# Optimization experiments

Hardware: AMD Instinct MI355X
Metric: run time of the kernel (lower is better)

Reference implementation:

```python
import jax, jax.numpy as jnp
import numpy as np

DILATIONS = [2 ** i for i in range(10)] * 5  # dilation_depth=10, n_repeat=5 -> 50 layers
B, C_IN, L = 8, 256, 16384
N_RES, N_SKIP = 32, 512
FINAL_LEN = L - sum(DILATIONS)  # 16384 - 5115 = 11269 (valid causal convs shrink length)


def setup_inputs() -> dict:
    key = jax.random.key(0)
    ks = jax.random.split(key, 8)
    s = lambda k, shape, scale: jax.random.normal(k, shape, jnp.float32) * scale
    nl = len(DILATIONS)
    return {
        "x": s(ks[0], (B, C_IN, L), 1.0),
        "w_in": s(ks[1], (N_RES, C_IN, 1), 0.06),
        "b_in": jnp.zeros((N_RES,), jnp.float32),
        "w_sig": s(ks[2], (nl, N_RES, N_RES, 2), 0.12),
        "b_sig": jnp.zeros((nl, N_RES), jnp.float32),
        "w_tanh": s(ks[3], (nl, N_RES, N_RES, 2), 0.12),
        "b_tanh": jnp.zeros((nl, N_RES), jnp.float32),
        "w_skip": s(ks[4], (nl, N_SKIP, N_RES), 0.17),
        "b_skip": jnp.zeros((nl, N_SKIP), jnp.float32),
        "w_res": s(ks[5], (nl, N_RES, N_RES), 0.17),
        "b_res": jnp.zeros((nl, N_RES), jnp.float32),
        "w_post1": s(ks[6], (N_SKIP, N_SKIP, 1), 0.04),
        "b_post1": jnp.zeros((N_SKIP,), jnp.float32),
        "w_post2": s(ks[7], (C_IN, N_SKIP, 1), 0.04),
        "b_post2": jnp.zeros((C_IN,), jnp.float32),
    }


def _dconv(x, w, b, d):
    # valid (causal, no-pad) dilated conv1d; x: [B,C,L], w: [O,I,K]
    y = jax.lax.conv_general_dilated(
        x, w, window_strides=(1,), padding='VALID', rhs_dilation=(d,),
        dimension_numbers=('NCH', 'OIH', 'NCH'))
    return y + b[None, :, None]


def reference(x, w_in, b_in, w_sig, b_sig, w_tanh, b_tanh, w_skip, b_skip,
              w_res, b_res, w_post1, b_post1, w_post2, b_post2):
    out = _dconv(x, w_in, b_in, 1)  # [B, n_residue, L]
    skip_sum = jnp.zeros((x.shape[0], w_skip.shape[1], FINAL_LEN), x.dtype)
    for i, d in enumerate(DILATIONS):
        gate = jax.nn.sigmoid(_dconv(out, w_sig[i], b_sig[i], d)) \
             * jnp.tanh(_dconv(out, w_tanh[i], b_tanh[i], d))
        # 1x1 skip conv, immediately trimmed to the final length (same math as
        # torch's trim-at-the-end since only the last FINAL_LEN samples survive)
        skip = jnp.einsum('oc,bcl->bol', w_skip[i], gate[:, :, -FINAL_LEN:]) \
             + b_skip[i][None, :, None]
        skip_sum = skip_sum + skip
        res = jnp.einsum('oc,bcl->bol', w_res[i], gate) + b_res[i][None, :, None]
        out = res + out[:, :, -res.shape[2]:]
    h = jax.nn.elu(skip_sum)
    h = _dconv(h, w_post1, b_post1, 1)
    h = jax.nn.elu(h)
    return _dconv(h, w_post2, b_post2, 1)  # [B, 256, FINAL_LEN]
```

## Files before the change

### kernel.cpp

```cpp
#include <hip/hip_runtime.h>
#include <hip/hip_bf16.h>
#include <cstdio>
#include <cstdint>

#define BATCH 8
#define CIN 256
#define L0 16384
#define NRES 32
#define NSKIP 512
#define NL 50
#define FINAL_LEN 11269
#define NTROW 11392

typedef __attribute__((ext_vector_type(4))) float f32x4v;
typedef __attribute__((ext_vector_type(8))) short s16x8;
typedef __attribute__((ext_vector_type(4))) short s16x4;

__device__ __forceinline__ int SWS(int r, int s) {
    return s ^ (r & 3) ^ ((r >> 2) & 1);
}
__device__ __forceinline__ short f2bf(float f) {
    __hip_bfloat16 h = __float2bfloat16(f);
    return *reinterpret_cast<short*>(&h);
}
__device__ __forceinline__ void gload16(const void* g, void* l) {
    __builtin_amdgcn_global_load_lds(
        (const __attribute__((address_space(1))) unsigned int*)g,
        (__attribute__((address_space(3))) unsigned int*)l, 16, 0, 0);
}

__global__ void k_bias_sum(const float* __restrict__ b_skip, float* __restrict__ bsum) {
    int o = threadIdx.x;
    if (o < NSKIP) {
        float s = 0.f;
        for (int i = 0; i < NL; ++i) s += b_skip[i * NSKIP + o];
        bsum[o] = s;
    }
}

__global__ __launch_bounds__(256) void k_cvt_skip(const float* __restrict__ w, short* __restrict__ out) {
    int idx = blockIdx.x * 256 + threadIdx.x;
    if (idx >= NSKIP * NL) return;
    int o = idx % NSKIP, ly = idx / NSKIP;
    const float* src = w + ((size_t)ly * NSKIP + o) * NRES;
    size_t base = (size_t)o * (NL * NRES) + ly * NRES;
#pragma unroll
    for (int s = 0; s < 4; ++s) {
        s16x8 v;
#pragma unroll
        for (int j = 0; j < 8; ++j) v[j] = f2bf(src[s * 8 + j]);
        *reinterpret_cast<s16x8*>(out + base + SWS(o & 7, s) * 8) = v;
    }
}

__global__ __launch_bounds__(256) void k_cvt_mat(const float* __restrict__ w, short* __restrict__ out, int M) {
    int idx = blockIdx.x * 256 + threadIdx.x;
    if (idx >= M * 16) return;
    int m = idx >> 4, kc = idx & 15;
    const float* src = w + (size_t)m * 512 + kc * 32;
    size_t base = (size_t)m * 512 + kc * 32;
#pragma unroll
    for (int s = 0; s < 4; ++s) {
        s16x8 v;
#pragma unroll
        for (int j = 0; j < 8; ++j) v[j] = f2bf(src[s * 8 + j]);
        *reinterpret_cast<s16x8*>(out + base + SWS(m & 7, s) * 8) = v;
    }
}

__global__ __launch_bounds__(256) void k_cvt_w(
    const float* __restrict__ ws, const float* __restrict__ wt, const float* __restrict__ wr,
    short* __restrict__ Wc, short* __restrict__ Wres) {
    int idx = blockIdx.x * 256 + threadIdx.x;
    if (idx < NL * 64 * 64) {
        int k = idx & 63, o = (idx >> 6) & 63, i = idx >> 12;
        int c = k & 31, tap = k >> 5;
        float v = (o < 32) ? ws[((i * NRES + o) * NRES + c) * 2 + tap]
                           : wt[((i * NRES + (o - 32)) * NRES + c) * 2 + tap];
        Wc[idx] = f2bf(v);
    } else {
        int j = idx - NL * 64 * 64;
        if (j < NL * 32 * 32) Wres[j] = f2bf(wr[j]);
    }
}

__global__ __launch_bounds__(256) void k_zero_tail(short* __restrict__ gT) {
    int i = blockIdx.x * 256 + threadIdx.x;
    const int per_b = (NTROW - FINAL_LEN) * 200;
    if (i >= BATCH * per_b) return;
    int b = i / per_b, r = i % per_b;
    int row = FINAL_LEN + r / 200, c = r % 200;
    s16x8 z = {0, 0, 0, 0, 0, 0, 0, 0};
    *reinterpret_cast<s16x8*>(gT + ((size_t)b * NTROW + row) * (NL * NRES) + c * 8) = z;
}

__global__ __launch_bounds__(256) void k_conv_in(
    const float* __restrict__ x, const float* __restrict__ w,
    const float* __restrict__ bias, float* __restrict__ out, short* __restrict__ outH) {
    const int b = blockIdx.y;
    const int t = blockIdx.x * 256 + threadIdx.x;
    float acc[NRES];
#pragma unroll
    for (int o = 0; o < NRES; ++o) acc[o] = bias[o];
    const float* xp = x + (size_t)b * CIN * L0 + t;
    for (int c = 0; c < CIN; ++c) {
        float xv = xp[(size_t)c * L0];
#pragma unroll
        for (int o = 0; o < NRES; ++o) acc[o] = fmaf(w[o * CIN + c], xv, acc[o]);
    }
    float* op = out + (size_t)b * NRES * L0 + t;
#pragma unroll
    for (int o = 0; o < NRES; ++o) op[(size_t)o * L0] = acc[o];
    short* hp = outH + ((size_t)b * L0 + t) * NRES;
#pragma unroll
    for (int s = 0; s < 4; ++s) {
        s16x8 v;
#pragma unroll
        for (int j = 0; j < 8; ++j) v[j] = f2bf(acc[s * 8 + j]);
        *reinterpret_cast<s16x8*>(hp + s * 8) = v;
    }
}

__global__ __launch_bounds__(256) void k_layer_mfma(
    const float* __restrict__ srcF, const short* __restrict__ srcH,
    float* __restrict__ dstF, short* __restrict__ dstH,
    short* __restrict__ gout,
    const short* __restrict__ Wc,
    const short* __restrict__ Wr,
    const float* __restrict__ bsig, const float* __restrict__ btan,
    const float* __restrict__ bres, int d, int out_len) {
    const int tid = threadIdx.x;
    const int l = tid & 63, w = tid >> 6;
    const int lr = l & 15, lg = l >> 4;
    const int b = blockIdx.y;
    const int t0w = blockIdx.x * 256 + w * 64;
    const int t0g = out_len - FINAL_LEN;

    __shared__ short gsm[4][64][40];
    __shared__ short hsm[4][64][40];

    s16x8 aW[4][2];
#pragma unroll
    for (int mf = 0; mf < 4; ++mf)
#pragma unroll
        for (int kf = 0; kf < 2; ++kf)
            aW[mf][kf] = *reinterpret_cast<const s16x8*>(&Wc[(mf * 16 + lr) * 64 + kf * 32 + lg * 8]);
    s16x8 aR[2];
#pragma unroll
    for (int mf = 0; mf < 2; ++mf)
        aR[mf] = *reinterpret_cast<const s16x8*>(&Wr[(mf * 16 + lr) * 32 + lg * 8]);

    float bs[2][4], bt[2][4], br[2][4];
#pragma unroll
    for (int mf = 0; mf < 2; ++mf)
#pragma unroll
        for (int j = 0; j < 4; ++j) {
            int o = mf * 16 + lg * 4 + j;
            bs[mf][j] = bsig[o]; bt[mf][j] = btan[o]; br[mf][j] = bres[o];
        }

    const float* sF = srcF + (size_t)b * NRES * L0;
    const short* sH = srcH + (size_t)b * L0 * NRES;
    float* dF = dstF + (size_t)b * NRES * L0;

#pragma unroll 1
    for (int nf = 0; nf < 4; ++nf) {
        const int tl = nf * 16 + lr;
        const int t = t0w + tl;
        const int tc = t < out_len ? t : (out_len - 1);
        s16x8 bx0 = *reinterpret_cast<const s16x8*>(&sH[(size_t)tc * NRES + lg * 8]);
        s16x8 bx1 = *reinterpret_cast<const s16x8*>(&sH[(size_t)(tc + d) * NRES + lg * 8]);

        f32x4v acc[4];
#pragma unroll
        for (int mf = 0; mf < 4; ++mf) acc[mf] = {0.f, 0.f, 0.f, 0.f};
#pragma unroll
        for (int mf = 0; mf < 4; ++mf) {
            acc[mf] = __builtin_amdgcn_mfma_f32_16x16x32_bf16(aW[mf][0], bx0, acc[mf], 0, 0, 0);
            acc[mf] = __builtin_amdgcn_mfma_f32_16x16x32_bf16(aW[mf][1], bx1, acc[mf], 0, 0, 0);
        }

#pragma unroll
        for (int mf = 0; mf < 2; ++mf) {
            s16x4 gq;
#pragma unroll
            for (int j = 0; j < 4; ++j) {
                float Ps = acc[mf][j] + bs[mf][j];
                float Pt = acc[mf + 2][j] + bt[mf][j];
                float sg = 1.f / (1.f + __expf(-Ps));
                float e2 = __expf(2.f * Pt);
                float th = 1.f - 2.f / (e2 + 1.f);
                gq[j] = f2bf(sg * th);
            }
            *reinterpret_cast<s16x4*>(&gsm[w][tl][mf * 16 + lg * 4]) = gq;
        }
        __syncthreads();

        s16x8 bg = *reinterpret_cast<const s16x8*>(&gsm[w][tl][lg * 8]);
        f32x4v accR[2];
#pragma unroll
        for (int mf = 0; mf < 2; ++mf) {
            accR[mf] = {0.f, 0.f, 0.f, 0.f};
            accR[mf] = __builtin_amdgcn_mfma_f32_16x16x32_bf16(aR[mf], bg, accR[mf], 0, 0, 0);
        }

        if (t < out_len) {
#pragma unroll
            for (int mf = 0; mf < 2; ++mf) {
                s16x4 hq;
#pragma unroll
                for (int j = 0; j < 4; ++j) {
                    int o = mf * 16 + lg * 4 + j;
                    float v = accR[mf][j] + br[mf][j] + sF[(size_t)o * L0 + t + d];
                    dF[(size_t)o * L0 + t] = v;
                    hq[j] = f2bf(v);
                }
                *reinterpret_cast<s16x4*>(&hsm[w][tl][mf * 16 + lg * 4]) = hq;
            }
        }
    }
    __syncthreads();

    short* dH = dstH + (size_t)b * L0 * NRES;
#pragma unroll
    for (int k = 0; k < 4; ++k) {
        int r = k * 16 + (l >> 2);
        int t = t0w + r;
        int c = l & 3;
        if (t < out_len) {
            s16x8 hv = *reinterpret_cast<const s16x8*>(&hsm[w][r][c * 8]);
            *reinterpret_cast<s16x8*>(&dH[(size_t)t * NRES + c * 8]) = hv;
            if (t >= t0g) {
                int tg = t - t0g;
                s16x8 gv = *reinterpret_cast<const s16x8*>(&gsm[w][r][c * 8]);
                *reinterpret_cast<s16x8*>(
                    &gout[((size_t)b * NTROW + tg) * (NL * NRES) + SWS(tg & 7, c) * 8]) = gv;
            }
        }
    }
}

template <int KTOT, bool DOELU, int OUTMODE>
__global__ __launch_bounds__(256) void k_mm(
    const short* __restrict__ A, const float* __restrict__ bias,
    const short* __restrict__ B, short* __restrict__ outS,
    float* __restrict__ outF, int Mtot) {
    const int tid = threadIdx.x;
    const int l = tid & 63, w = tid >> 6;
    const int t0 = blockIdx.x * 128;
    const int m0 = blockIdx.y * 128;
    const int bb = blockIdx.z;

    __shared__ __attribute__((aligned(16))) char Asm_[2][8192];
    __shared__ __attribute__((aligned(16))) char Bsm_[2][8192];

    const char* Ag = (const char*)A;
    const char* Bg = (const char*)B + (size_t)bb * NTROW * (KTOT * 2);

    const int rstage = w * 16 + (l >> 2);
    const char* a0 = Ag + (size_t)(m0 + rstage) * (KTOT * 2) + (l & 3) * 16;
    const char* a1 = a0 + (size_t)64 * (KTOT * 2);
    const char* b0 = Bg + (size_t)(t0 + rstage) * (KTOT * 2) + (l & 3) * 16;
    const char* b1 = b0 + (size_t)64 * (KTOT * 2);

    const int wm = (w >> 1) * 64, wn = (w & 1) * 64;
    const int slotSw = ((l >> 4) ^ (l & 3) ^ ((l >> 2) & 1)) * 16;
    const int aoff = (wm + (l & 15)) * 64 + slotSw;
    const int boff = (wn + (l & 15)) * 64 + slotSw;

    f32x4v acc[4][4];
#pragma unroll
    for (int i = 0; i < 4; ++i)
#pragma unroll
        for (int j = 0; j < 4; ++j) acc[i][j] = {0.f, 0.f, 0.f, 0.f};

    constexpr int NKT = KTOT / 32;
    gload16(a0, &Asm_[0][w * 1024]);
    gload16(a1, &Asm_[0][4096 + w * 1024]);
    gload16(b0, &Bsm_[0][w * 1024]);
    gload16(b1, &Bsm_[0][4096 + w * 1024]);
    __syncthreads();

    for (int kt = 0; kt < NKT; ++kt) {
        const int cur = kt & 1;
        if (kt + 1 < NKT) {
            size_t ko = (size_t)(kt + 1) * 64;
            gload16(a0 + ko, &Asm_[cur ^ 1][w * 1024]);
            gload16(a1 + ko, &Asm_[cur ^ 1][4096 + w * 1024]);
            gload16(b0 + ko, &Bsm_[cur ^ 1][w * 1024]);
            gload16(b1 + ko, &Bsm_[cur ^ 1][4096 + w * 1024]);
        }
        s16x8 af[4], bf_[4];
#pragma unroll
        for (int i = 0; i < 4; ++i)
            af[i] = *reinterpret_cast<const s16x8*>(&Asm_[cur][aoff + i * 1024]);
#pragma unroll
        for (int i = 0; i < 4; ++i)
            bf_[i] = *reinterpret_cast<const s16x8*>(&Bsm_[cur][boff + i * 1024]);
#pragma unroll
        for (int i = 0; i < 4; ++i)
#pragma unroll
            for (int j = 0; j < 4; ++j)
                acc[i][j] = __builtin_amdgcn_mfma_f32_16x16x32_bf16(af[i], bf_[j], acc[i][j], 0, 0, 0);
        __syncthreads();
    }

    const int colc = l & 15;
    const int rowc = (l >> 4) * 4;
#pragma unroll
    for (int mf = 0; mf < 4; ++mf) {
        const int ch = m0 + wm + mf * 16 + rowc;
        const float4 bv = *reinterpret_cast<const float4*>(&bias[ch]);
        const float* bvp = (const float*)&bv;
#pragma unroll
        for (int nf = 0; nf < 4; ++nf) {
            const int t = t0 + wn + nf * 16 + colc;
            float vb[4];
#pragma unroll
            for (int j = 0; j < 4; ++j) {
                float v = acc[mf][nf][j] + bvp[j];
                if (DOELU) v = v > 0.f ? v : (__expf(v) - 1.f);
                vb[j] = v;
            }
            if (OUTMODE == 0) {
                s16x4 pv;
#pragma unroll
                for (int j = 0; j < 4; ++j) pv[j] = f2bf(vb[j]);
                size_t el = ((size_t)bb * NTROW + t) * 512 + (ch >> 5) * 32
                          + SWS(t & 7, (ch >> 3) & 3) * 8 + (ch & 7);
                *reinterpret_cast<s16x4*>(outS + el) = pv;
            } else {
                if (t < FINAL_LEN) {
#pragma unroll
                    for (int j = 0; j < 4; ++j)
                        outF[((size_t)bb * Mtot + ch + j) * FINAL_LEN + t] = vb[j];
                }
            }
        }
    }
}

extern "C" void kernel_launch(void* const* d_in, const int* in_sizes, int n_in,
                              void* d_out, int out_size, void* d_ws, size_t ws_size,
                              hipStream_t stream) {
    const float* x      = (const float*)d_in[0];
    const float* w_in   = (const float*)d_in[1];
    const float* b_in   = (const float*)d_in[2];
    const float* w_sig  = (const float*)d_in[3];
    const float* b_sig  = (const float*)d_in[4];
    const float* w_tanh = (const float*)d_in[5];
    const float* b_tanh = (const float*)d_in[6];
    const float* w_skip = (const float*)d_in[7];
    const float* b_skip = (const float*)d_in[8];
    const float* w_res  = (const float*)d_in[9];
    const float* b_res  = (const float*)d_in[10];
    const float* w_p1   = (const float*)d_in[11];
    const float* b_p1   = (const float*)d_in[12];
    const float* w_p2   = (const float*)d_in[13];
    const float* b_p2   = (const float*)d_in[14];
    float* out = (float*)d_out;

    float* bufA   = (float*)d_ws;
    float* bufB   = bufA + (size_t)BATCH * NRES * L0;
    float* bsum   = bufB + (size_t)BATCH * NRES * L0;
    short* Askip  = (short*)(bsum + NSKIP);
    short* Ap1    = Askip + (size_t)NSKIP * NL * NRES;
    short* Ap2    = Ap1 + (size_t)NSKIP * NSKIP;
    short* WcH    = Ap2 + (size_t)CIN * NSKIP;
    short* WresH  = WcH + (size_t)NL * 64 * 64;
    short* gatesT = WresH + (size_t)NL * 32 * 32;
    short* hbufT  = gatesT + (size_t)BATCH * NTROW * (NL * NRES);
    short* h2bufT = gatesT;
    short* shadowA = hbufT;
    short* shadowB = shadowA + (size_t)BATCH * L0 * NRES;

    size_t need = (size_t)((char*)(hbufT + (size_t)BATCH * NTROW * NSKIP) - (char*)d_ws);
    if (ws_size < need)
        fprintf(stderr, "WS TOO SMALL: have %zu need %zu\n", ws_size, need);

    k_bias_sum<<<1, 512, 0, stream>>>(b_skip, bsum);
    k_cvt_skip<<<(NSKIP * NL + 255) / 256, 256, 0, stream>>>(w_skip, Askip);
    k_cvt_mat<<<(NSKIP * 16 + 255) / 256, 256, 0, stream>>>(w_p1, Ap1, NSKIP);
    k_cvt_mat<<<(CIN * 16 + 255) / 256, 256, 0, stream>>>(w_p2, Ap2, CIN);
    k_cvt_w<<<(NL * 64 * 64 + NL * 32 * 32 + 255) / 256, 256, 0, stream>>>(
        w_sig, w_tanh, w_res, WcH, WresH);
    k_zero_tail<<<(BATCH * (NTROW - FINAL_LEN) * 200 + 255) / 256, 256, 0, stream>>>(gatesT);
    k_conv_in<<<dim3(L0 / 256, BATCH), 256, 0, stream>>>(x, w_in, b_in, bufA, shadowA);

    float* srcF = bufA;  float* dstF = bufB;
    short* srcH = shadowA; short* dstH = shadowB;
    int len = L0;
    for (int i = 0; i < NL; ++i) {
        int d = 1 << (i % 10);
        int out_len = len - d;
        dim3 grid((out_len + 255) / 256, BATCH);
        k_layer_mfma<<<grid, 256, 0, stream>>>(
            srcF, srcH, dstF, dstH, gatesT + (size_t)i * NRES,
            WcH + (size_t)i * 4096, WresH + (size_t)i * 1024,
            b_sig + i * 32, b_tanh + i * 32, b_res + i * 32, d, out_len);
        float* tf = srcF; srcF = dstF; dstF = tf;
        short* th = srcH; srcH = dstH; dstH = th;
        len = out_len;
    }

    k_mm<1600, true, 0><<<dim3(89, 4, BATCH), 256, 0, stream>>>(Askip, bsum, gatesT, hbufT, nullptr, NSKIP);
    k_mm<512,  true, 0><<<dim3(89, 4, BATCH), 256, 0, stream>>>(Ap1, b_p1, hbufT, h2bufT, nullptr, NSKIP);
    k_mm<512, false, 1><<<dim3(89, 2, BATCH), 256, 0, stream>>>(Ap2, b_p2, h2bufT, nullptr, out, CIN);
}
```

Before: 1.623 ms.

## Fuse all residual layers into one persistent kernel with grid barriers

Replaces the fifty per-layer launches with a single persistent kernel of 512 blocks that loops over layers and synchronises through a global atomic barrier. The residual stream becomes a time-major fp32 buffer that is converted to bf16 on the fly, which removes the separate bf16 shadow copy and its writes. The per-warp __syncthreads is replaced by an LDS waitcnt, and the k_mm grids are remapped to a swizzled 1D tile order meant to improve cache reuse. The gains come from lower launch overhead and less memory traffic. The risks are spin-wait cost at each barrier, a possible deadlock if not all 512 blocks are co-resident (the barrier breaks out after a bounded number of spins), and uneven work because each block handles one fixed tile.

```diff
diff --git a/kernel.cpp b/kernel.cpp
--- a/kernel.cpp
+++ b/kernel.cpp
@@ -11,6 +11,7 @@
 #define NL 50
 #define FINAL_LEN 11269
 #define NTROW 11392
+#define NBLK 512
 
 typedef __attribute__((ext_vector_type(4))) float f32x4v;
 typedef __attribute__((ext_vector_type(8))) short s16x8;
@@ -27,6 +28,23 @@
     __builtin_amdgcn_global_load_lds(
         (const __attribute__((address_space(1))) unsigned int*)g,
         (__attribute__((address_space(3))) unsigned int*)l, 16, 0, 0);
+}
+
+__global__ void k_init_bar(int* c) { if (threadIdx.x < 64) c[threadIdx.x] = 0; }
+
+__device__ __forceinline__ void gbarrier(int* cnt, int target) {
+    __syncthreads();
+    if (threadIdx.x == 0) {
+        __threadfence();
+        __hip_atomic_fetch_add(cnt, 1, __ATOMIC_RELEASE, __HIP_MEMORY_SCOPE_AGENT);
+        int it = 0;
+        while (__hip_atomic_load(cnt, __ATOMIC_ACQUIRE, __HIP_MEMORY_SCOPE_AGENT) < target) {
+            __builtin_amdgcn_s_sleep(2);
+            if (++it > (1 << 20)) break;
+        }
+        __threadfence();
+    }
+    __syncthreads();
 }
 
 __global__ void k_bias_sum(const float* __restrict__ b_skip, float* __restrict__ bsum) {
@@ -96,7 +114,7 @@
 
 __global__ __launch_bounds__(256) void k_conv_in(
     const float* __restrict__ x, const float* __restrict__ w,
-    const float* __restrict__ bias, float* __restrict__ out, short* __restrict__ outH) {
+    const float* __restrict__ bias, float* __restrict__ outT) {
     const int b = blockIdx.y;
     const int t = blockIdx.x * 256 + threadIdx.x;
     float acc[NRES];
@@ -108,147 +126,162 @@
 #pragma unroll
         for (int o = 0; o < NRES; ++o) acc[o] = fmaf(w[o * CIN + c], xv, acc[o]);
     }
-    float* op = out + (size_t)b * NRES * L0 + t;
-#pragma unroll
-    for (int o = 0; o < NRES; ++o) op[(size_t)o * L0] = acc[o];
-    short* hp = outH + ((size_t)b * L0 + t) * NRES;
-#pragma unroll
-    for (int s = 0; s < 4; ++s) {
-        s16x8 v;
-#pragma unroll
-        for (int j = 0; j < 8; ++j) v[j] = f2bf(acc[s * 8 + j]);
-        *reinterpret_cast<s16x8*>(hp + s * 8) = v;
-    }
-}
-
-__global__ __launch_bounds__(256) void k_layer_mfma(
-    const float* __restrict__ srcF, const short* __restrict__ srcH,
-    float* __restrict__ dstF, short* __restrict__ dstH,
-    short* __restrict__ gout,
-    const short* __restrict__ Wc,
-    const short* __restrict__ Wr,
-    const float* __restrict__ bsig, const float* __restrict__ btan,
-    const float* __restrict__ bres, int d, int out_len) {
+    float* op = outT + ((size_t)b * L0 + t) * NRES;
+#pragma unroll
+    for (int s = 0; s < 8; ++s) {
+        f32x4v v = {acc[s * 4], acc[s * 4 + 1], acc[s * 4 + 2], acc[s * 4 + 3]};
+        *reinterpret_cast<f32x4v*>(op + s * 4) = v;
+    }
+}
+
+__global__ __launch_bounds__(256, 2) void k_layers_all(
+    float* __restrict__ bufA, float* __restrict__ bufB,
+    short* __restrict__ gatesT,
+    const short* __restrict__ WcAll, const short* __restrict__ WrAll,
+    const float* __restrict__ bsigAll, const float* __restrict__ btanAll,
+    const float* __restrict__ bresAll, int* __restrict__ barcnt) {
     const int tid = threadIdx.x;
-    const int l = tid & 63, w = tid >> 6;
+    const int l = tid & 63, wv = tid >> 6;
     const int lr = l & 15, lg = l >> 4;
-    const int b = blockIdx.y;
-    const int t0w = blockIdx.x * 256 + w * 64;
-    const int t0g = out_len - FINAL_LEN;
+    const int bid = blockIdx.x;
+    const int tx = bid >> 3, b = bid & 7;
 
     __shared__ short gsm[4][64][40];
-    __shared__ short hsm[4][64][40];
-
-    s16x8 aW[4][2];
-#pragma unroll
-    for (int mf = 0; mf < 4; ++mf)
-#pragma unroll
-        for (int kf = 0; kf < 2; ++kf)
-            aW[mf][kf] = *reinterpret_cast<const s16x8*>(&Wc[(mf * 16 + lr) * 64 + kf * 32 + lg * 8]);
-    s16x8 aR[2];
-#pragma unroll
-    for (int mf = 0; mf < 2; ++mf)
-        aR[mf] = *reinterpret_cast<const s16x8*>(&Wr[(mf * 16 + lr) * 32 + lg * 8]);
-
-    float bs[2][4], bt[2][4], br[2][4];
-#pragma unroll
-    for (int mf = 0; mf < 2; ++mf)
-#pragma unroll
-        for (int j = 0; j < 4; ++j) {
-            int o = mf * 16 + lg * 4 + j;
-            bs[mf][j] = bsig[o]; bt[mf][j] = btan[o]; br[mf][j] = bres[o];
-        }
-
-    const float* sF = srcF + (size_t)b * NRES * L0;
-    const short* sH = srcH + (size_t)b * L0 * NRES;
-    float* dF = dstF + (size_t)b * NRES * L0;
-
-#pragma unroll 1
-    for (int nf = 0; nf < 4; ++nf) {
-        const int tl = nf * 16 + lr;
-        const int t = t0w + tl;
-        const int tc = t < out_len ? t : (out_len - 1);
-        s16x8 bx0 = *reinterpret_cast<const s16x8*>(&sH[(size_t)tc * NRES + lg * 8]);
-        s16x8 bx1 = *reinterpret_cast<const s16x8*>(&sH[(size_t)(tc + d) * NRES + lg * 8]);
-
-        f32x4v acc[4];
-#pragma unroll
-        for (int mf = 0; mf < 4; ++mf) acc[mf] = {0.f, 0.f, 0.f, 0.f};
-#pragma unroll
-        for (int mf = 0; mf < 4; ++mf) {
-            acc[mf] = __builtin_amdgcn_mfma_f32_16x16x32_bf16(aW[mf][0], bx0, acc[mf], 0, 0, 0);
-            acc[mf] = __builtin_amdgcn_mfma_f32_16x16x32_bf16(aW[mf][1], bx1, acc[mf], 0, 0, 0);
-        }
-
-#pragma unroll
-        for (int mf = 0; mf < 2; ++mf) {
-            s16x4 gq;
-#pragma unroll
-            for (int j = 0; j < 4; ++j) {
-                float Ps = acc[mf][j] + bs[mf][j];
-                float Pt = acc[mf + 2][j] + bt[mf][j];
-                float sg = 1.f / (1.f + __expf(-Ps));
-                float e2 = __expf(2.f * Pt);
-                float th = 1.f - 2.f / (e2 + 1.f);
-                gq[j] = f2bf(sg * th);
-            }
-            *reinterpret_cast<s16x4*>(&gsm[w][tl][mf * 16 + lg * 4]) = gq;
-        }
-        __syncthreads();
-
-        s16x8 bg = *reinterpret_cast<const s16x8*>(&gsm[w][tl][lg * 8]);
-        f32x4v accR[2];
-#pragma unroll
-        for (int mf = 0; mf < 2; ++mf) {
-            accR[mf] = {0.f, 0.f, 0.f, 0.f};
-            accR[mf] = __builtin_amdgcn_mfma_f32_16x16x32_bf16(aR[mf], bg, accR[mf], 0, 0, 0);
-        }
-
-        if (t < out_len) {
-#pragma unroll
-            for (int mf = 0; mf < 2; ++mf) {
-                s16x4 hq;
+
+    float* sF = bufA;
+    float* dF = bufB;
+    int len = L0;
+
+    for (int i = 0; i < NL; ++i) {
+        const int d = 1 << (i % 10);
+        const int out_len = len - d;
+        const int tiles = (out_len + 255) >> 8;
+
+        if (tx < tiles) {
+            const short* Wc = WcAll + (size_t)i * 4096;
+            const short* Wr = WrAll + (size_t)i * 1024;
+            s16x8 aW[4][2], aR[2];
+#pragma unroll
+            for (int mf = 0; mf < 4; ++mf)
+#pragma unroll
+                for (int kf = 0; kf < 2; ++kf)
+                    aW[mf][kf] = *reinterpret_cast<const s16x8*>(&Wc[(mf * 16 + lr) * 64 + kf * 32 + lg * 8]);
+#pragma unroll
+            for (int mf = 0; mf < 2; ++mf)
+                aR[mf] = *reinterpret_cast<const s16x8*>(&Wr[(mf * 16 + lr) * 32 + lg * 8]);
+
+            float bs2[2][4], bt2[2][4], br2[2][4];
+#pragma unroll
+            for (int mf = 0; mf < 2; ++mf)
 #pragma unroll
                 for (int j = 0; j < 4; ++j) {
                     int o = mf * 16 + lg * 4 + j;
-                    float v = accR[mf][j] + br[mf][j] + sF[(size_t)o * L0 + t + d];
-                    dF[(size_t)o * L0 + t] = v;
-                    hq[j] = f2bf(v);
-                }
-                *reinterpret_cast<s16x4*>(&hsm[w][tl][mf * 16 + lg * 4]) = hq;
+                    bs2[mf][j] = bsigAll[i * 32 + o];
+                    bt2[mf][j] = btanAll[i * 32 + o];
+                    br2[mf][j] = bresAll[i * 32 + o];
+                }
+
+            const float* sFb = sF + (size_t)b * L0 * NRES;
+            float* dFb = dF + (size_t)b * L0 * NRES;
+            short* go = gatesT + (size_t)i * NRES + (size_t)b * NTROW * (NL * NRES);
+            const int t0w = tx * 256 + wv * 64;
+            const int t0g = out_len - FINAL_LEN;
+
+#pragma unroll 1
+            for (int nf = 0; nf < 4; ++nf) {
+                const int tl = nf * 16 + lr;
+                const int t = t0w + tl;
+                const int tc = t < out_len ? t : (out_len - 1);
+                f32x4v x0a = *reinterpret_cast<const f32x4v*>(&sFb[(size_t)tc * NRES + lg * 8]);
+                f32x4v x0b = *reinterpret_cast<const f32x4v*>(&sFb[(size_t)tc * NRES + lg * 8 + 4]);
+                f32x4v x1a = *reinterpret_cast<const f32x4v*>(&sFb[(size_t)(tc + d) * NRES + lg * 8]);
+                f32x4v x1b = *reinterpret_cast<const f32x4v*>(&sFb[(size_t)(tc + d) * NRES + lg * 8 + 4]);
+                s16x8 bx0, bx1;
+#pragma unroll
+                for (int j = 0; j < 4; ++j) {
+                    bx0[j] = f2bf(x0a[j]); bx0[4 + j] = f2bf(x0b[j]);
+                    bx1[j] = f2bf(x1a[j]); bx1[4 + j] = f2bf(x1b[j]);
+                }
+
+                f32x4v acc[4];
+#pragma unroll
+                for (int mf = 0; mf < 4; ++mf) acc[mf] = {0.f, 0.f, 0.f, 0.f};
+#pragma unroll
+                for (int mf = 0; mf < 4; ++mf) {
+                    acc[mf] = __builtin_amdgcn_mfma_f32_16x16x32_bf16(aW[mf][0], bx0, acc[mf], 0, 0, 0);
+                    acc[mf] = __builtin_amdgcn_mfma_f32_16x16x32_bf16(aW[mf][1], bx1, acc[mf], 0, 0, 0);
+                }
+
+#pragma unroll
+                for (int mf = 0; mf < 2; ++mf) {
+                    s16x4 gq;
+#pragma unroll
+                    for (int j = 0; j < 4; ++j) {
+                        float Ps = acc[mf][j] + bs2[mf][j];
+                        float Pt = acc[mf + 2][j] + bt2[mf][j];
+                        float sg = 1.f / (1.f + __expf(-Ps));
+                        float e2 = __expf(2.f * Pt);
+                        float th = 1.f - 2.f / (e2 + 1.f);
+                        gq[j] = f2bf(sg * th);
+                    }
+                    *reinterpret_cast<s16x4*>(&gsm[wv][tl][mf * 16 + lg * 4]) = gq;
+                }
+                asm volatile("s_waitcnt lgkmcnt(0)" ::: "memory");
+
+                s16x8 bg = *reinterpret_cast<const s16x8*>(&gsm[wv][tl][lg * 8]);
+                f32x4v accR[2];
+#pragma unroll
+                for (int mf = 0; mf < 2; ++mf) {
+                    accR[mf] = {0.f, 0.f, 0.f, 0.f};
+                    accR[mf] = __builtin_amdgcn_mfma_f32_16x16x32_bf16(aR[mf], bg, accR[mf], 0, 0, 0);
+                }
+
+                if (t < out_len) {
+#pragma unroll
+                    for (int mf = 0; mf < 2; ++mf) {
+                        f32x4v rv = *reinterpret_cast<const f32x4v*>(&sFb[(size_t)(t + d) * NRES + mf * 16 + lg * 4]);
+                        f32x4v ov;
+#pragma unroll
+                        for (int j = 0; j < 4; ++j) ov[j] = accR[mf][j] + br2[mf][j] + rv[j];
+                        *reinterpret_cast<f32x4v*>(&dFb[(size_t)t * NRES + mf * 16 + lg * 4]) = ov;
+                    }
+                }
+            }
+            asm volatile("s_waitcnt lgkmcnt(0)" ::: "memory");
+
+#pragma unroll
+            for (int k = 0; k < 4; ++k) {
+                int r = k * 16 + (l >> 2);
+                int t = t0w + r;
+                int c = l & 3;
+                if (t >= t0g && t < out_len) {
+                    int tg = t - t0g;
+                    s16x8 gv = *reinterpret_cast<const s16x8*>(&gsm[wv][r][c * 8]);
+                    *reinterpret_cast<s16x8*>(&go[(size_t)tg * (NL * NRES) + SWS(tg & 7, c) * 8]) = gv;
+                }
             }
         }
-    }
-    __syncthreads();
-
-    short* dH = dstH + (size_t)b * L0 * NRES;
-#pragma unroll
-    for (int k = 0; k < 4; ++k) {
-        int r = k * 16 + (l >> 2);
-        int t = t0w + r;
-        int c = l & 3;
-        if (t < out_len) {
-            s16x8 hv = *reinterpret_cast<const s16x8*>(&hsm[w][r][c * 8]);
-            *reinterpret_cast<s16x8*>(&dH[(size_t)t * NRES + c * 8]) = hv;
-            if (t >= t0g) {
-                int tg = t - t0g;
-                s16x8 gv = *reinterpret_cast<const s16x8*>(&gsm[w][r][c * 8]);
-                *reinterpret_cast<s16x8*>(
-                    &gout[((size_t)b * NTROW + tg) * (NL * NRES) + SWS(tg & 7, c) * 8]) = gv;
-            }
-        }
-    }
-}
-
-template <int KTOT, bool DOELU, int OUTMODE>
+
+        if (i + 1 < NL) gbarrier(barcnt, NBLK * (i + 1));
+        float* tf = sF; sF = dF; dF = tf;
+        len = out_len;
+    }
+}
+
+template <int KTOT, bool DOELU, int OUTMODE, int NM>
 __global__ __launch_bounds__(256) void k_mm(
     const short* __restrict__ A, const float* __restrict__ bias,
     const short* __restrict__ B, short* __restrict__ outS,
     float* __restrict__ outF, int Mtot) {
     const int tid = threadIdx.x;
     const int l = tid & 63, w = tid >> 6;
-    const int t0 = blockIdx.x * 128;
-    const int m0 = blockIdx.y * 128;
+
+    const int id = blockIdx.x;
+    const int rr = id % (8 * NM);
+    const int ttile = (id / (8 * NM)) * 8 + (rr & 7);
+    if (ttile >= NTROW / 128) return;
+    const int t0 = ttile * 128;
+    const int m0 = (rr >> 3) * 128;
     const int bb = blockIdx.z;
 
     __shared__ __attribute__((aligned(16))) char Asm_[2][8192];
@@ -371,10 +404,9 @@
     short* gatesT = WresH + (size_t)NL * 32 * 32;
     short* hbufT  = gatesT + (size_t)BATCH * NTROW * (NL * NRES);
     short* h2bufT = gatesT;
-    short* shadowA = hbufT;
-    short* shadowB = shadowA + (size_t)BATCH * L0 * NRES;
-
-    size_t need = (size_t)((char*)(hbufT + (size_t)BATCH * NTROW * NSKIP) - (char*)d_ws);
+    int*   barcnt = (int*)(hbufT + (size_t)BATCH * NTROW * NSKIP);
+
+    size_t need = (size_t)((char*)(barcnt + 64) - (char*)d_ws);
     if (ws_size < need)
         fprintf(stderr, "WS TOO SMALL: have %zu need %zu\n", ws_size, need);
 
@@ -385,25 +417,13 @@
     k_cvt_w<<<(NL * 64 * 64 + NL * 32 * 32 + 255) / 256, 256, 0, stream>>>(
         w_sig, w_tanh, w_res, WcH, WresH);
     k_zero_tail<<<(BATCH * (NTROW - FINAL_LEN) * 200 + 255) / 256, 256, 0, stream>>>(gatesT);
-    k_conv_in<<<dim3(L0 / 256, BATCH), 256, 0, stream>>>(x, w_in, b_in, bufA, shadowA);
-
-    float* srcF = bufA;  float* dstF = bufB;
-    short* srcH = shadowA; short* dstH = shadowB;
-    int len = L0;
-    for (int i = 0; i < NL; ++i) {
-        int d = 1 << (i % 10);
-        int out_len = len - d;
-        dim3 grid((out_len + 255) / 256, BATCH);
-        k_layer_mfma<<<grid, 256, 0, stream>>>(
-            srcF, srcH, dstF, dstH, gatesT + (size_t)i * NRES,
-            WcH + (size_t)i * 4096, WresH + (size_t)i * 1024,
-            b_sig + i * 32, b_tanh + i * 32, b_res + i * 32, d, out_len);
-        float* tf = srcF; srcF = dstF; dstF = tf;
-        short* th = srcH; srcH = dstH; dstH = th;
-        len = out_len;
-    }
-
-    k_mm<1600, true, 0><<<dim3(89, 4, BATCH), 256, 0, stream>>>(Askip, bsum, gatesT, hbufT, nullptr, NSKIP);
-    k_mm<512,  true, 0><<<dim3(89, 4, BATCH), 256, 0, stream>>>(Ap1, b_p1, hbufT, h2bufT, nullptr, NSKIP);
-    k_mm<512, false, 1><<<dim3(89, 2, BATCH), 256, 0, stream>>>(Ap2, b_p2, h2bufT, nullptr, out, CIN);
-}
+    k_init_bar<<<1, 64, 0, stream>>>(barcnt);
+    k_conv_in<<<dim3(L0 / 256, BATCH), 256, 0, stream>>>(x, w_in, b_in, bufA);
+
+    k_layers_all<<<NBLK, 256, 0, stream>>>(
+        bufA, bufB, gatesT, WcH, WresH, b_sig, b_tanh, b_res, barcnt);
+
+    k_mm<1600, true, 0, 4><<<dim3(384, 1, BATCH), 256, 0, stream>>>(Askip, bsum, gatesT, hbufT, nullptr, NSKIP);
+    k_mm<512,  true, 0, 4><<<dim3(384, 1, BATCH), 256, 0, stream>>>(Ap1, b_p1, hbufT, h2bufT, nullptr, NSKIP);
+    k_mm<512, false, 1, 2><<<dim3(192, 1, BATCH), 256, 0, stream>>>(Ap2, b_p2, h2bufT, nullptr, out, CIN);
+}
```

Result: slower. 5.321 ms (+227.9%).
